# Kernel tuning notes

Measured on AMD Instinct MI355X. Metric: run time of the kernel, lower is better.

Reference implementation:

```python
import jax, jax.numpy as jnp
import numpy as np

N, E = 100000, 1600000
DIMS = [128, 64, 64, 64, 32]  # in, hid, hid, hid, out
NEG_SLOPE = 0.2               # GATv2Conv default negative_slope
ELU_ALPHA_OUT = float(DIMS[-1])  # nn.ELU(out_channels): alpha = out_channels


def setup_inputs() -> dict:
    key = jax.random.key(0)
    ks = jax.random.split(key, 16)
    inp = {
        "x": jax.random.normal(ks[0], (N, DIMS[0]), dtype=jnp.float32),
        "edge_index": jax.random.randint(ks[1], (2, E), 0, N, dtype=jnp.int64),
    }
    ki = 2
    for i in range(4):
        fin, fout = DIMS[i], DIMS[i + 1]
        s = 1.0 / np.sqrt(fin)
        inp[f"Wl{i+1}"] = jax.random.uniform(ks[ki], (fin, fout), jnp.float32, -s, s); ki += 1
        inp[f"Wr{i+1}"] = jax.random.uniform(ks[ki], (fin, fout), jnp.float32, -s, s); ki += 1
        inp[f"att{i+1}"] = jax.random.uniform(ks[ki], (fout,), jnp.float32, -s, s); ki += 1
    return inp


def gatv2_layer(x, src, dst, Wl, Wr, att):
    # single head, concat=False, no self-loops, no bias (per module config)
    xl = x @ Wl                                   # [N, F] source-side projection
    xr = x @ Wr                                   # [N, F] target-side projection
    e = jax.nn.leaky_relu(xl[src] + xr[dst], NEG_SLOPE)   # [E, F]
    score = e @ att                               # [E]
    # softmax over incoming edges of each destination node
    m = jax.ops.segment_max(score, dst, num_segments=N)    # [N]
    ex = jnp.exp(score - m[dst])                  # [E]
    denom = jax.ops.segment_sum(ex, dst, num_segments=N)   # [N]
    alpha = ex / (denom[dst] + 1e-16)             # [E]
    # scatter-add weighted source messages
    return jax.ops.segment_sum(xl[src] * alpha[:, None], dst, num_segments=N)


def reference(x, edge_index, Wl1, Wr1, att1, Wl2, Wr2, att2, Wl3, Wr3, att3, Wl4, Wr4, att4):
    src, dst = edge_index[0], edge_index[1]
    h = jax.nn.elu(gatv2_layer(x, src, dst, Wl1, Wr1, att1))
    h = jax.nn.elu(gatv2_layer(h, src, dst, Wl2, Wr2, att2))
    h = jax.nn.elu(gatv2_layer(h, src, dst, Wl3, Wr3, att3))
    h = gatv2_layer(h, src, dst, Wl4, Wr4, att4)
    # nn.ELU(out_channels) -> ELU with alpha = out_channels (faithful quirk)
    return jnp.where(h > 0, h, ELU_ALPHA_OUT * jnp.expm1(h))
```

## Files before the change

### kernel.cpp

```cpp
#include <hip/hip_runtime.h>
#include <math.h>

typedef __attribute__((ext_vector_type(8))) short bf16x8;
typedef __attribute__((ext_vector_type(4))) float f32x4;
typedef __attribute__((ext_vector_type(2))) _Float16 h2;

#define BSHIFT 7
#define CH 8192

__device__ inline unsigned short f32_to_bf16_bits(float f) {
    unsigned int u = __float_as_uint(f);
    unsigned int r = (u + 0x7fffu + ((u >> 16) & 1u)) >> 16;
    return (unsigned short)r;
}
__device__ inline float bf16_bits_to_f32(unsigned short h) {
    return __uint_as_float(((unsigned int)h) << 16);
}
__device__ inline h2 u2h(unsigned u) { return __builtin_bit_cast(h2, u); }
__device__ inline unsigned h2u(h2 h) { return __builtin_bit_cast(unsigned, h); }

#define SWZ_ADD(t, imm) \
    t += __int_as_float(__builtin_amdgcn_ds_swizzle(__float_as_int(t), imm))

__device__ inline float dot2acc(h2 a, h2 b, float c) {
#if defined(__has_builtin)
#if __has_builtin(__builtin_amdgcn_fdot2)
    return __builtin_amdgcn_fdot2(a, b, c, false);
#else
    return c + (float)a[0] * (float)b[0] + (float)a[1] * (float)b[1];
#endif
#else
    return c + (float)a[0] * (float)b[0] + (float)a[1] * (float)b[1];
#endif
}


__global__ __launch_bounds__(256) void bucket_hist(
    const int* __restrict__ dst, int* __restrict__ bcnt8, int E, int nb, int nbp)
{
    __shared__ int h[1024];
    for (int i = threadIdx.x; i < nb; i += 256) h[i] = 0;
    __syncthreads();
    int e0 = blockIdx.x * CH, e1 = min(e0 + CH, E);
    for (int e = e0 + (int)threadIdx.x; e < e1; e += 256)
        atomicAdd(&h[dst[e] >> BSHIFT], 1);
    __syncthreads();
    int* mycnt = bcnt8 + (blockIdx.x & 7) * nbp;
    for (int b = threadIdx.x; b < nb; b += 256) {
        int c = h[b];
        if (c) atomicAdd(&mycnt[b], c);
    }
}

__global__ void bucket_scan(const int* __restrict__ bcnt8, int* __restrict__ bbase,
                            int* __restrict__ bcur8, int* __restrict__ rowstart,
                            int nb, int nbp, int E, int N)
{
    __shared__ int sh[1024];
    int t = threadIdx.x;
    int g8[8];
    int tot = 0;
#pragma unroll
    for (int g = 0; g < 8; ++g) {
        int c = (t < nb) ? bcnt8[g * nbp + t] : 0;
        g8[g] = c; tot += c;
    }
    sh[t] = tot;
    __syncthreads();
    for (int d = 1; d < 1024; d <<= 1) {
        int a = (t >= d) ? sh[t - d] : 0;
        __syncthreads();
        sh[t] += a;
        __syncthreads();
    }
    int base = sh[t] - tot;
    if (t <= nb) bbase[t] = base;
    if (t < nb) {
        int run = base;
#pragma unroll
        for (int g = 0; g < 8; ++g) { bcur8[g * nbp + t] = run; run += g8[g]; }
    }
    if (t == 0) rowstart[N] = E;
}

__global__ __launch_bounds__(256) void bucket_scatter(
    const int* __restrict__ src, const int* __restrict__ dst,
    int* __restrict__ bcur8, unsigned* __restrict__ pairs, int E, int nb, int nbp)
{
    __shared__ int h[1024];
    for (int i = threadIdx.x; i < nb; i += 256) h[i] = 0;
    __syncthreads();
    int e0 = blockIdx.x * CH, e1 = min(e0 + CH, E);
    for (int e = e0 + (int)threadIdx.x; e < e1; e += 256)
        atomicAdd(&h[dst[e] >> BSHIFT], 1);
    __syncthreads();
    int* mycur = bcur8 + (blockIdx.x & 7) * nbp;
    for (int b = threadIdx.x; b < nb; b += 256) {
        int c = h[b];
        if (c) h[b] = atomicAdd(&mycur[b], c);
    }
    __syncthreads();
    for (int e = e0 + (int)threadIdx.x; e < e1; e += 256) {
        int d = dst[e];
        int pos = atomicAdd(&h[d >> BSHIFT], 1);
        pairs[pos] = ((unsigned)src[e] << BSHIFT) | (unsigned)(d & 127);
    }
}

__global__ __launch_bounds__(256) void bucket_finalize(
    const unsigned* __restrict__ pairs, const int* __restrict__ bbase,
    int* __restrict__ rowstart, int* __restrict__ csr_src, int N)
{
    __shared__ int h[128];
    __shared__ int sh[256];
    int b = blockIdx.x;
    int p0 = bbase[b], p1 = bbase[b + 1];
    int t = threadIdx.x;
    if (t < 128) h[t] = 0;
    __syncthreads();
    for (int e = p0 + t; e < p1; e += 256)
        atomicAdd(&h[pairs[e] & 127], 1);
    __syncthreads();
    int v = (t < 128) ? h[t] : 0;
    sh[t] = v;
    __syncthreads();
    for (int d = 1; d < 256; d <<= 1) {
        int a = (t >= d) ? sh[t - d] : 0;
        __syncthreads();
        sh[t] += a;
        __syncthreads();
    }
    if (t < 128) {
        int off = sh[t] - v;
        int node = (b << BSHIFT) + t;
        if (node < N) rowstart[node] = p0 + off;
        h[t] = p0 + off;
    }
    __syncthreads();
    for (int e = p0 + t; e < p1; e += 256) {
        unsigned pr = pairs[e];
        int pos = atomicAdd(&h[pr & 127], 1);
        csr_src[pos] = (int)(pr >> BSHIFT);
    }
}


__global__ void prepack_kernel(const float* __restrict__ Wl, const float* __restrict__ Wr,
                               unsigned short* __restrict__ pWl, unsigned short* __restrict__ pWr,
                               int FIN, int FOUT) {
    int NT = FOUT >> 4, NK = FIN >> 5;
    int part = NT * NK * 512;
    int i = blockIdx.x * blockDim.x + threadIdx.x;
    int m = i / part;
    if (m >= 2) return;
    int ii = i - m * part;
    int j = ii & 7;
    int lane = (ii >> 3) & 63;
    int rest = ii >> 9;
    int ks = rest % NK;
    int t = rest / NK;
    int k = ks * 32 + (lane >> 4) * 8 + j;
    int c = t * 16 + (lane & 15);
    const float* W = m ? Wr : Wl;
    unsigned short* P = m ? pWr : pWl;
    float w = W[(size_t)k * FOUT + c];
    unsigned short hi = f32_to_bf16_bits(w);
    unsigned short lo = f32_to_bf16_bits(w - bf16_bits_to_f32(hi));
    P[ii] = hi;
    P[part + ii] = lo;
}


template<int FIN, int FOUT>
__global__ __launch_bounds__(256) void proj_mfma_kernel(
    const float* __restrict__ x,
    const unsigned short* __restrict__ pWl, const unsigned short* __restrict__ pWr,
    const float* __restrict__ att,
    _Float16* __restrict__ xlh, _Float16* __restrict__ xrh,
    float* __restrict__ dl, float* __restrict__ dr, int n)
{
    constexpr int NT = FOUT >> 4;
    constexpr int NK = FIN >> 5;
    constexpr int PART = NT * NK * 512;
    const int wave = threadIdx.x >> 6;
    const int lane = threadIdx.x & 63;
    const int row0 = blockIdx.x * 64 + wave * 16;
    int arow = row0 + (lane & 15);
    if (arow >= n) arow = n - 1;
    const int khalf = lane >> 4;

    f32x4 accl[NT], accr[NT];
#pragma unroll
    for (int t = 0; t < NT; ++t) {
        accl[t] = (f32x4){0.f, 0.f, 0.f, 0.f};
        accr[t] = (f32x4){0.f, 0.f, 0.f, 0.f};
    }

    const float* xrow = x + (size_t)arow * FIN + khalf * 8;
#pragma unroll
    for (int ks = 0; ks < NK; ++ks) {
        float4 a0 = *(const float4*)(xrow + ks * 32);
        float4 a1 = *(const float4*)(xrow + ks * 32 + 4);
        float av[8] = {a0.x, a0.y, a0.z, a0.w, a1.x, a1.y, a1.z, a1.w};
        bf16x8 ah, al;
#pragma unroll
        for (int j = 0; j < 8; ++j) {
            unsigned short h = f32_to_bf16_bits(av[j]);
            ah[j] = (short)h;
            al[j] = (short)f32_to_bf16_bits(av[j] - bf16_bits_to_f32(h));
        }
#pragma unroll
        for (int t = 0; t < NT; ++t) {
            const unsigned short* bpl = pWl + ((size_t)(t * NK + ks) * 64 + lane) * 8;
            bf16x8 bh  = *(const bf16x8*)bpl;
            bf16x8 blo = *(const bf16x8*)(bpl + PART);
            accl[t] = __builtin_amdgcn_mfma_f32_16x16x32_bf16(ah, bh,  accl[t], 0, 0, 0);
            accl[t] = __builtin_amdgcn_mfma_f32_16x16x32_bf16(ah, blo, accl[t], 0, 0, 0);
            accl[t] = __builtin_amdgcn_mfma_f32_16x16x32_bf16(al, bh,  accl[t], 0, 0, 0);
            const unsigned short* bpr = pWr + ((size_t)(t * NK + ks) * 64 + lane) * 8;
            bh  = *(const bf16x8*)bpr;
            blo = *(const bf16x8*)(bpr + PART);
            accr[t] = __builtin_amdgcn_mfma_f32_16x16x32_bf16(ah, bh,  accr[t], 0, 0, 0);
            accr[t] = __builtin_amdgcn_mfma_f32_16x16x32_bf16(ah, blo, accr[t], 0, 0, 0);
            accr[t] = __builtin_amdgcn_mfma_f32_16x16x32_bf16(al, bh,  accr[t], 0, 0, 0);
        }
    }

    const int orow0 = row0 + khalf * 4;
    const int colb = lane & 15;
    float attc[NT];
#pragma unroll
    for (int t = 0; t < NT; ++t) attc[t] = att[t * 16 + colb];

#pragma unroll
    for (int t = 0; t < NT; ++t) {
        int col = t * 16 + colb;
#pragma unroll
        for (int r = 0; r < 4; ++r) {
            int rr = orow0 + r;
            if (rr < n) {
                xlh[(size_t)rr * FOUT + col] = (_Float16)accl[t][r];
                xrh[(size_t)rr * FOUT + col] = (_Float16)accr[t][r];
            }
        }
    }
#pragma unroll
    for (int r = 0; r < 4; ++r) {
        float pl = 0.f, pr = 0.f;
#pragma unroll
        for (int t = 0; t < NT; ++t) { pl += accl[t][r] * attc[t]; pr += accr[t][r] * attc[t]; }
#pragma unroll
        for (int off = 1; off < 16; off <<= 1) {
            pl += __shfl_xor(pl, off);
            pr += __shfl_xor(pr, off);
        }
        int rr = orow0 + r;
        if (colb == 0 && rr < n) { dl[rr] = pl; dr[rr] = pr; }
    }
}


template<int F, int AMODE>
__global__ __launch_bounds__(256) void agg_kernel(
    const _Float16* __restrict__ xlh, const _Float16* __restrict__ xrh,
    const float* __restrict__ att,
    const float* __restrict__ dl, const float* __restrict__ dr,
    const int* __restrict__ rowstart, const int* __restrict__ csr_src,
    float* __restrict__ out, int n, int E)
{
    constexpr int LPE = F / 8;
    constexpr int LSH = (F == 64) ? 6 : 5;
    constexpr int NPG = 64 / LPE;

    int wv  = (blockIdx.x * blockDim.x + threadIdx.x) >> 6;
    int lane = threadIdx.x & 63;
    int grp = lane / LPE;
    int fl  = lane % LPE;
    int node = wv * NPG + grp;
    bool act = node < n;
    int nc = act ? node : 0;

    float4 xrraw = *(const float4*)(xrh + (((unsigned)nc << LSH) + fl * 8));
    h2 xrv[4];
#pragma unroll
    for (int j = 0; j < 4; ++j) xrv[j] = u2h(((const unsigned*)&xrraw)[j]);
    h2 atth[4];
#pragma unroll
    for (int j = 0; j < 4; ++j) {
        atth[j][0] = (_Float16)att[fl * 8 + 2 * j];
        atth[j][1] = (_Float16)att[fl * 8 + 2 * j + 1];
    }
    float cdr = 0.6f * dr[nc];

    int s0 = rowstart[nc];
    int s1 = act ? rowstart[nc + 1] : s0;
    int s1c = min(max(s1 - 1, s0), E - 1);

    float m = -1e30f, mth = -1e30f, ssum = 0.f;
    float o[8];
#pragma unroll
    for (int j = 0; j < 8; ++j) o[j] = 0.f;

    int ia = s0, ib = s0 + 1;
    int sva = csr_src[min(ia, s1c)];
    int svb = csr_src[min(ib, s1c)];
    float dla = dl[sva], dlb = dl[svb];
    float4 rawa = *(const float4*)(xlh + (((unsigned)sva << LSH) + fl * 8));
    float4 rawb = *(const float4*)(xlh + (((unsigned)svb << LSH) + fl * 8));

    while (ia < s1) {
        int nia = ia + 2, nib = ib + 2;
        int nsva = csr_src[min(nia, s1c)];
        int nsvb = csr_src[min(nib, s1c)];
        float ndla = dl[nsva], ndlb = dl[nsvb];
        float4 nrawa = *(const float4*)(xlh + (((unsigned)nsva << LSH) + fl * 8));
        float4 nrawb = *(const float4*)(xlh + (((unsigned)nsvb << LSH) + fl * 8));

        h2 a[4], b[4];
#pragma unroll
        for (int j = 0; j < 4; ++j) {
            a[j] = u2h(((const unsigned*)&rawa)[j]);
            b[j] = u2h(((const unsigned*)&rawb)[j]);
        }

        bool vb = ib < s1;
        float ta = 0.f, tb = 0.f;
#pragma unroll
        for (int j = 0; j < 4; ++j) {
            h2 ea = a[j] + xrv[j];
            h2 eb = b[j] + xrv[j];
            ea = u2h(h2u(ea) & 0x7FFF7FFFu);
            eb = u2h(h2u(eb) & 0x7FFF7FFFu);
            ta = dot2acc(atth[j], ea, ta);
            tb = dot2acc(atth[j], eb, tb);
        }
        SWZ_ADD(ta, 0x041F); SWZ_ADD(tb, 0x041F);
        SWZ_ADD(ta, 0x081F); SWZ_ADD(tb, 0x081F);
        if (LPE == 8) { SWZ_ADD(ta, 0x101F); SWZ_ADD(tb, 0x101F); }

        float pa = 0.6f * dla + cdr + 0.4f * ta;
        float pb = vb ? (0.6f * dlb + cdr + 0.4f * tb) : -1e30f;

        float pm = fmaxf(pa, pb);
        if (pm > mth) {
            float c = __expf(m - pm);
            ssum *= c;
#pragma unroll
            for (int j = 0; j < 8; ++j) o[j] *= c;
            m = pm; mth = pm + 8.0f;
        }
        float wa = __expf(pa - m);
        float wb = __expf(pb - m);
        ssum += wa + wb;
#pragma unroll
        for (int j = 0; j < 4; ++j) {
            o[2 * j]     += wa * (float)a[j][0] + wb * (float)b[j][0];
            o[2 * j + 1] += wa * (float)a[j][1] + wb * (float)b[j][1];
        }

        ia = nia; ib = nib;
        dla = ndla; dlb = ndlb; rawa = nrawa; rawb = nrawb;
    }

    float inv = 1.f / (ssum + 1e-16f);
    float res[8];
#pragma unroll
    for (int j = 0; j < 8; ++j) {
        float r = o[j] * inv;
        if (AMODE == 1) r = (r > 0.f) ? r : expm1f(r);
        else            r = (r > 0.f) ? r : 32.f * expm1f(r);
        res[j] = r;
    }
    if (act) {
        float* op = out + (((unsigned)node << LSH) + fl * 8);
        *(float4*)op       = (float4){res[0], res[1], res[2], res[3]};
        *(float4*)(op + 4) = (float4){res[4], res[5], res[6], res[7]};
    }
}


extern "C" void kernel_launch(void* const* d_in, const int* in_sizes, int n_in,
                              void* d_out, int out_size, void* d_ws, size_t ws_size,
                              hipStream_t stream) {
    const float* x    = (const float*)d_in[0];
    const int*   ei   = (const int*)d_in[1];
    const float* Wl1  = (const float*)d_in[2];
    const float* Wr1  = (const float*)d_in[3];
    const float* att1 = (const float*)d_in[4];
    const float* Wl2  = (const float*)d_in[5];
    const float* Wr2  = (const float*)d_in[6];
    const float* att2 = (const float*)d_in[7];
    const float* Wl3  = (const float*)d_in[8];
    const float* Wr3  = (const float*)d_in[9];
    const float* att3 = (const float*)d_in[10];
    const float* Wl4  = (const float*)d_in[11];
    const float* Wr4  = (const float*)d_in[12];
    const float* att4 = (const float*)d_in[13];

    const int N = in_sizes[0] / 128;
    const int E = in_sizes[1] / 2;
    const int* src = ei;
    const int* dst = ei + E;

    const int nb  = (N + 127) >> BSHIFT;
    const int nbp = (nb + 15) & ~15;

    char* w = (char*)d_ws;
    size_t off = 0;
    auto take = [&](size_t bytes) -> void* {
        void* p = w + off;
        off = (off + bytes + 255) & ~(size_t)255;
        return p;
    };
    int* bcnt8    = (int*)take((size_t)8 * nbp * 4);
    int* bcur8    = (int*)take((size_t)8 * nbp * 4);
    int* bbase    = (int*)take((size_t)(nb + 1) * 4);
    int* rowstart = (int*)take((size_t)(N + 1) * 4);
    int* csr_src  = (int*)take((size_t)E * 4);
    float* dl = (float*)take((size_t)N * 4);
    float* dr = (float*)take((size_t)N * 4);
    _Float16* xlh = (_Float16*)take((size_t)N * 64 * 2);
    _Float16* xrh = (_Float16*)take((size_t)N * 64 * 2);
    float* hA = (float*)take((size_t)N * 64 * 4);
    float* hB = (float*)take((size_t)N * 64 * 4);
    unsigned short* pWl1 = (unsigned short*)take(2 * 4 * 4 * 512 * 2);
    unsigned short* pWr1 = (unsigned short*)take(2 * 4 * 4 * 512 * 2);
    unsigned short* pWl2 = (unsigned short*)take(2 * 4 * 2 * 512 * 2);
    unsigned short* pWr2 = (unsigned short*)take(2 * 4 * 2 * 512 * 2);
    unsigned short* pWl3 = (unsigned short*)take(2 * 4 * 2 * 512 * 2);
    unsigned short* pWr3 = (unsigned short*)take(2 * 4 * 2 * 512 * 2);
    unsigned short* pWl4 = (unsigned short*)take(2 * 2 * 2 * 512 * 2);
    unsigned short* pWr4 = (unsigned short*)take(2 * 2 * 2 * 512 * 2);
    unsigned* pairs = (unsigned*)hA;
    float* outf = (float*)d_out;

    hipMemsetAsync(bcnt8, 0, (size_t)8 * nbp * 4, stream);

    prepack_kernel<<<(2 * 4 * 4 * 512 + 255) / 256, 256, 0, stream>>>(Wl1, Wr1, pWl1, pWr1, 128, 64);
    prepack_kernel<<<(2 * 4 * 2 * 512 + 255) / 256, 256, 0, stream>>>(Wl2, Wr2, pWl2, pWr2, 64, 64);
    prepack_kernel<<<(2 * 4 * 2 * 512 + 255) / 256, 256, 0, stream>>>(Wl3, Wr3, pWl3, pWr3, 64, 64);
    prepack_kernel<<<(2 * 2 * 2 * 512 + 255) / 256, 256, 0, stream>>>(Wl4, Wr4, pWl4, pWr4, 64, 32);

    int kgrid = (E + CH - 1) / CH;
    bucket_hist<<<kgrid, 256, 0, stream>>>(dst, bcnt8, E, nb, nbp);
    bucket_scan<<<1, 1024, 0, stream>>>(bcnt8, bbase, bcur8, rowstart, nb, nbp, E, N);
    bucket_scatter<<<kgrid, 256, 0, stream>>>(src, dst, bcur8, pairs, E, nb, nbp);
    bucket_finalize<<<nb, 256, 0, stream>>>(pairs, bbase, rowstart, csr_src, N);

    int pblk = (N + 63) / 64;
    int agg64 = (N + 31) / 32;
    int agg32 = (N + 63) / 64;

    proj_mfma_kernel<128, 64><<<pblk, 256, 0, stream>>>(x, pWl1, pWr1, att1, xlh, xrh, dl, dr, N);
    agg_kernel<64, 1><<<agg64, 256, 0, stream>>>(xlh, xrh, att1, dl, dr, rowstart, csr_src, hA, N, E);

    proj_mfma_kernel<64, 64><<<pblk, 256, 0, stream>>>(hA, pWl2, pWr2, att2, xlh, xrh, dl, dr, N);
    agg_kernel<64, 1><<<agg64, 256, 0, stream>>>(xlh, xrh, att2, dl, dr, rowstart, csr_src, hB, N, E);

    proj_mfma_kernel<64, 64><<<pblk, 256, 0, stream>>>(hB, pWl3, pWr3, att3, xlh, xrh, dl, dr, N);
    agg_kernel<64, 1><<<agg64, 256, 0, stream>>>(xlh, xrh, att3, dl, dr, rowstart, csr_src, hA, N, E);

    proj_mfma_kernel<64, 32><<<pblk, 256, 0, stream>>>(hA, pWl4, pWr4, att4, xlh, xrh, dl, dr, N);
    agg_kernel<32, 2><<<agg32, 256, 0, stream>>>(xlh, xrh, att4, dl, dr, rowstart, csr_src, outf, N, E);
}
```

Baseline: 304.6 us.

## Sort aggregation nodes by in-degree and deepen edge gather prefetch

Adds a counting sort of nodes by in-degree (histogram, scan, scatter) and has each aggregation wave process nodes in that permuted order. Nodes sharing a wave then have similar edge counts, which reduces lane divergence in the per-node edge loop. The edge loop also prefetches two edge pairs ahead instead of one, to hide gather latency. In exchange it adds three small preprocessing kernels and an indirection, and writes to the output and reads of per-node data become non-contiguous. The deeper prefetch also raises register pressure.

```diff
diff --git a/kernel.cpp b/kernel.cpp
--- a/kernel.cpp
+++ b/kernel.cpp
@@ -141,6 +141,37 @@
         unsigned pr = pairs[e];
         int pos = atomicAdd(&h[pr & 127], 1);
         csr_src[pos] = (int)(pr >> BSHIFT);
+    }
+}
+
+
+__global__ void deg_hist(const int* __restrict__ rowstart, int* __restrict__ dhist, int N) {
+    int i = blockIdx.x * blockDim.x + threadIdx.x;
+    if (i < N) atomicAdd(&dhist[min(rowstart[i + 1] - rowstart[i], 255)], 1);
+}
+
+__global__ void deg_scan(const int* __restrict__ dhist, int* __restrict__ dcur) {
+    __shared__ int sh[256];
+    int t = threadIdx.x;
+    int v = dhist[t];
+    sh[t] = v;
+    __syncthreads();
+    for (int d = 1; d < 256; d <<= 1) {
+        int a = (t >= d) ? sh[t - d] : 0;
+        __syncthreads();
+        sh[t] += a;
+        __syncthreads();
+    }
+    dcur[t] = sh[t] - v;
+}
+
+__global__ void deg_scatter(const int* __restrict__ rowstart, int* __restrict__ dcur,
+                            int* __restrict__ perm, int N) {
+    int i = blockIdx.x * blockDim.x + threadIdx.x;
+    if (i < N) {
+        int d = min(rowstart[i + 1] - rowstart[i], 255);
+        int r = atomicAdd(&dcur[d], 1);
+        perm[r] = i;
     }
 }
 
@@ -266,6 +297,7 @@
     const float* __restrict__ att,
     const float* __restrict__ dl, const float* __restrict__ dr,
     const int* __restrict__ rowstart, const int* __restrict__ csr_src,
+    const int* __restrict__ perm,
     float* __restrict__ out, int n, int E)
 {
     constexpr int LPE = F / 8;
@@ -276,11 +308,11 @@
     int lane = threadIdx.x & 63;
     int grp = lane / LPE;
     int fl  = lane % LPE;
-    int node = wv * NPG + grp;
-    bool act = node < n;
-    int nc = act ? node : 0;
-
-    float4 xrraw = *(const float4*)(xrh + (((unsigned)nc << LSH) + fl * 8));
+    int idx = wv * NPG + grp;
+    bool act = idx < n;
+    int node = act ? perm[idx] : 0;
+
+    float4 xrraw = *(const float4*)(xrh + (((unsigned)node << LSH) + fl * 8));
     h2 xrv[4];
 #pragma unroll
     for (int j = 0; j < 4; ++j) xrv[j] = u2h(((const unsigned*)&xrraw)[j]);
@@ -290,10 +322,10 @@
         atth[j][0] = (_Float16)att[fl * 8 + 2 * j];
         atth[j][1] = (_Float16)att[fl * 8 + 2 * j + 1];
     }
-    float cdr = 0.6f * dr[nc];
-
-    int s0 = rowstart[nc];
-    int s1 = act ? rowstart[nc + 1] : s0;
+    float cdr = 0.6f * dr[node];
+
+    int s0 = rowstart[node];
+    int s1 = act ? rowstart[node + 1] : s0;
     int s1c = min(max(s1 - 1, s0), E - 1);
 
     float m = -1e30f, mth = -1e30f, ssum = 0.f;
@@ -301,29 +333,34 @@
 #pragma unroll
     for (int j = 0; j < 8; ++j) o[j] = 0.f;
 
-    int ia = s0, ib = s0 + 1;
-    int sva = csr_src[min(ia, s1c)];
-    int svb = csr_src[min(ib, s1c)];
-    float dla = dl[sva], dlb = dl[svb];
-    float4 rawa = *(const float4*)(xlh + (((unsigned)sva << LSH) + fl * 8));
-    float4 rawb = *(const float4*)(xlh + (((unsigned)svb << LSH) + fl * 8));
-
-    while (ia < s1) {
-        int nia = ia + 2, nib = ib + 2;
-        int nsva = csr_src[min(nia, s1c)];
-        int nsvb = csr_src[min(nib, s1c)];
-        float ndla = dl[nsva], ndlb = dl[nsvb];
-        float4 nrawa = *(const float4*)(xlh + (((unsigned)nsva << LSH) + fl * 8));
-        float4 nrawb = *(const float4*)(xlh + (((unsigned)nsvb << LSH) + fl * 8));
+    int i0 = s0;
+    int sa = csr_src[min(s0,     s1c)];
+    int sb = csr_src[min(s0 + 1, s1c)];
+    float da0 = dl[sa], db0 = dl[sb];
+    float4 ra0 = *(const float4*)(xlh + (((unsigned)sa << LSH) + fl * 8));
+    float4 rb0 = *(const float4*)(xlh + (((unsigned)sb << LSH) + fl * 8));
+    sa = csr_src[min(s0 + 2, s1c)];
+    sb = csr_src[min(s0 + 3, s1c)];
+    float da1 = dl[sa], db1 = dl[sb];
+    float4 ra1 = *(const float4*)(xlh + (((unsigned)sa << LSH) + fl * 8));
+    float4 rb1 = *(const float4*)(xlh + (((unsigned)sb << LSH) + fl * 8));
+
+    while (i0 < s1) {
+        int p2 = i0 + 4;
+        int sa2 = csr_src[min(p2,     s1c)];
+        int sb2 = csr_src[min(p2 + 1, s1c)];
+        float da2 = dl[sa2], db2 = dl[sb2];
+        float4 ra2 = *(const float4*)(xlh + (((unsigned)sa2 << LSH) + fl * 8));
+        float4 rb2 = *(const float4*)(xlh + (((unsigned)sb2 << LSH) + fl * 8));
 
         h2 a[4], b[4];
 #pragma unroll
         for (int j = 0; j < 4; ++j) {
-            a[j] = u2h(((const unsigned*)&rawa)[j]);
-            b[j] = u2h(((const unsigned*)&rawb)[j]);
-        }
-
-        bool vb = ib < s1;
+            a[j] = u2h(((const unsigned*)&ra0)[j]);
+            b[j] = u2h(((const unsigned*)&rb0)[j]);
+        }
+
+        bool vb = (i0 + 1) < s1;
         float ta = 0.f, tb = 0.f;
 #pragma unroll
         for (int j = 0; j < 4; ++j) {
@@ -338,8 +375,8 @@
         SWZ_ADD(ta, 0x081F); SWZ_ADD(tb, 0x081F);
         if (LPE == 8) { SWZ_ADD(ta, 0x101F); SWZ_ADD(tb, 0x101F); }
 
-        float pa = 0.6f * dla + cdr + 0.4f * ta;
-        float pb = vb ? (0.6f * dlb + cdr + 0.4f * tb) : -1e30f;
+        float pa = 0.6f * da0 + cdr + 0.4f * ta;
+        float pb = vb ? (0.6f * db0 + cdr + 0.4f * tb) : -1e30f;
 
         float pm = fmaxf(pa, pb);
         if (pm > mth) {
@@ -358,8 +395,9 @@
             o[2 * j + 1] += wa * (float)a[j][1] + wb * (float)b[j][1];
         }
 
-        ia = nia; ib = nib;
-        dla = ndla; dlb = ndlb; rawa = nrawa; rawb = nrawb;
+        i0 += 2;
+        da0 = da1; db0 = db1; ra0 = ra1; rb0 = rb1;
+        da1 = da2; db1 = db2; ra1 = ra2; rb1 = rb2;
     }
 
     float inv = 1.f / (ssum + 1e-16f);
@@ -417,6 +455,9 @@
     int* bbase    = (int*)take((size_t)(nb + 1) * 4);
     int* rowstart = (int*)take((size_t)(N + 1) * 4);
     int* csr_src  = (int*)take((size_t)E * 4);
+    int* dhist    = (int*)take(256 * 4);
+    int* dcur     = (int*)take(256 * 4);
+    int* perm     = (int*)take((size_t)N * 4);
     float* dl = (float*)take((size_t)N * 4);
     float* dr = (float*)take((size_t)N * 4);
     _Float16* xlh = (_Float16*)take((size_t)N * 64 * 2);
@@ -435,6 +476,7 @@
     float* outf = (float*)d_out;
 
     hipMemsetAsync(bcnt8, 0, (size_t)8 * nbp * 4, stream);
+    hipMemsetAsync(dhist, 0, 256 * 4, stream);
 
     prepack_kernel<<<(2 * 4 * 4 * 512 + 255) / 256, 256, 0, stream>>>(Wl1, Wr1, pWl1, pWr1, 128, 64);
     prepack_kernel<<<(2 * 4 * 2 * 512 + 255) / 256, 256, 0, stream>>>(Wl2, Wr2, pWl2, pWr2, 64, 64);
@@ -447,19 +489,24 @@
     bucket_scatter<<<kgrid, 256, 0, stream>>>(src, dst, bcur8, pairs, E, nb, nbp);
     bucket_finalize<<<nb, 256, 0, stream>>>(pairs, bbase, rowstart, csr_src, N);
 
+    int ngrid = (N + 255) / 256;
+    deg_hist<<<ngrid, 256, 0, stream>>>(rowstart, dhist, N);
+    deg_scan<<<1, 256, 0, stream>>>(dhist, dcur);
+    deg_scatter<<<ngrid, 256, 0, stream>>>(rowstart, dcur, perm, N);
+
     int pblk = (N + 63) / 64;
     int agg64 = (N + 31) / 32;
     int agg32 = (N + 63) / 64;
 
     proj_mfma_kernel<128, 64><<<pblk, 256, 0, stream>>>(x, pWl1, pWr1, att1, xlh, xrh, dl, dr, N);
-    agg_kernel<64, 1><<<agg64, 256, 0, stream>>>(xlh, xrh, att1, dl, dr, rowstart, csr_src, hA, N, E);
+    agg_kernel<64, 1><<<agg64, 256, 0, stream>>>(xlh, xrh, att1, dl, dr, rowstart, csr_src, perm, hA, N, E);
 
     proj_mfma_kernel<64, 64><<<pblk, 256, 0, stream>>>(hA, pWl2, pWr2, att2, xlh, xrh, dl, dr, N);
-    agg_kernel<64, 1><<<agg64, 256, 0, stream>>>(xlh, xrh, att2, dl, dr, rowstart, csr_src, hB, N, E);
+    agg_kernel<64, 1><<<agg64, 256, 0, stream>>>(xlh, xrh, att2, dl, dr, rowstart, csr_src, perm, hB, N, E);
 
     proj_mfma_kernel<64, 64><<<pblk, 256, 0, stream>>>(hB, pWl3, pWr3, att3, xlh, xrh, dl, dr, N);
-    agg_kernel<64, 1><<<agg64, 256, 0, stream>>>(xlh, xrh, att3, dl, dr, rowstart, csr_src, hA, N, E);
+    agg_kernel<64, 1><<<agg64, 256, 0, stream>>>(xlh, xrh, att3, dl, dr, rowstart, csr_src, perm, hA, N, E);
 
     proj_mfma_kernel<64, 32><<<pblk, 256, 0, stream>>>(hA, pWl4, pWr4, att4, xlh, xrh, dl, dr, N);
-    agg_kernel<32, 2><<<agg32, 256, 0, stream>>>(xlh, xrh, att4, dl, dr, rowstart, csr_src, outf, N, E);
-}
+    agg_kernel<32, 2><<<agg32, 256, 0, stream>>>(xlh, xrh, att4, dl, dr, rowstart, csr_src, perm, outf, N, E);
+}
```

After: 845.3 us. +177.5%, slower.

## Deepen gather prefetch pipeline in GAT aggregation loop to two stages

Applied to the files above, without the earlier changes.

Restructures the per-destination edge loop into a software pipeline that keeps two pairs of gathered source rows in flight and prefetches CSR source indices further ahead. The aim is to hide the latency of the dependent index-then-row gather chain behind the attention and softmax arithmetic. In exchange it uses more registers, which may reduce occupancy, and it issues more speculative clamped loads for nodes with few edges.

```diff
diff --git a/kernel.cpp b/kernel.cpp
--- a/kernel.cpp
+++ b/kernel.cpp
@@ -301,66 +301,89 @@
 #pragma unroll
     for (int j = 0; j < 8; ++j) o[j] = 0.f;
 
-    int ia = s0, ib = s0 + 1;
-    int sva = csr_src[min(ia, s1c)];
-    int svb = csr_src[min(ib, s1c)];
-    float dla = dl[sva], dlb = dl[svb];
-    float4 rawa = *(const float4*)(xlh + (((unsigned)sva << LSH) + fl * 8));
-    float4 rawb = *(const float4*)(xlh + (((unsigned)svb << LSH) + fl * 8));
-
-    while (ia < s1) {
-        int nia = ia + 2, nib = ib + 2;
-        int nsva = csr_src[min(nia, s1c)];
-        int nsvb = csr_src[min(nib, s1c)];
-        float ndla = dl[nsva], ndlb = dl[nsvb];
-        float4 nrawa = *(const float4*)(xlh + (((unsigned)nsva << LSH) + fl * 8));
-        float4 nrawb = *(const float4*)(xlh + (((unsigned)nsvb << LSH) + fl * 8));
-
-        h2 a[4], b[4];
-#pragma unroll
-        for (int j = 0; j < 4; ++j) {
-            a[j] = u2h(((const unsigned*)&rawa)[j]);
-            b[j] = u2h(((const unsigned*)&rawb)[j]);
-        }
-
-        bool vb = ib < s1;
-        float ta = 0.f, tb = 0.f;
-#pragma unroll
-        for (int j = 0; j < 4; ++j) {
-            h2 ea = a[j] + xrv[j];
-            h2 eb = b[j] + xrv[j];
-            ea = u2h(h2u(ea) & 0x7FFF7FFFu);
-            eb = u2h(h2u(eb) & 0x7FFF7FFFu);
-            ta = dot2acc(atth[j], ea, ta);
-            tb = dot2acc(atth[j], eb, tb);
-        }
-        SWZ_ADD(ta, 0x041F); SWZ_ADD(tb, 0x041F);
-        SWZ_ADD(ta, 0x081F); SWZ_ADD(tb, 0x081F);
-        if (LPE == 8) { SWZ_ADD(ta, 0x101F); SWZ_ADD(tb, 0x101F); }
-
-        float pa = 0.6f * dla + cdr + 0.4f * ta;
-        float pb = vb ? (0.6f * dlb + cdr + 0.4f * tb) : -1e30f;
-
-        float pm = fmaxf(pa, pb);
-        if (pm > mth) {
-            float c = __expf(m - pm);
-            ssum *= c;
-#pragma unroll
-            for (int j = 0; j < 8; ++j) o[j] *= c;
-            m = pm; mth = pm + 8.0f;
-        }
-        float wa = __expf(pa - m);
-        float wb = __expf(pb - m);
-        ssum += wa + wb;
-#pragma unroll
-        for (int j = 0; j < 4; ++j) {
-            o[2 * j]     += wa * (float)a[j][0] + wb * (float)b[j][0];
-            o[2 * j + 1] += wa * (float)a[j][1] + wb * (float)b[j][1];
-        }
-
-        ia = nia; ib = nib;
-        dla = ndla; dlb = ndlb; rawa = nrawa; rawb = nrawb;
-    }
+    int cA0 = csr_src[min(s0,     s1c)];
+    int cB0 = csr_src[min(s0 + 1, s1c)];
+    int cA1 = csr_src[min(s0 + 2, s1c)];
+    int cB1 = csr_src[min(s0 + 3, s1c)];
+    float4 rA0 = *(const float4*)(xlh + (((unsigned)cA0 << LSH) + fl * 8));
+    float4 rB0 = *(const float4*)(xlh + (((unsigned)cB0 << LSH) + fl * 8));
+    float  dA0 = dl[cA0], dB0 = dl[cB0];
+    float4 rA1 = *(const float4*)(xlh + (((unsigned)cA1 << LSH) + fl * 8));
+    float4 rB1 = *(const float4*)(xlh + (((unsigned)cB1 << LSH) + fl * 8));
+    float  dA1 = dl[cA1], dB1 = dl[cB1];
+    int fA0 = csr_src[min(s0 + 4, s1c)];
+    int fB0 = csr_src[min(s0 + 5, s1c)];
+    int fA1 = csr_src[min(s0 + 6, s1c)];
+    int fB1 = csr_src[min(s0 + 7, s1c)];
+
+    int i0 = s0;
+
+#define AGG_COMPUTE(RA, RB, DA, DB)                                          \
+    {                                                                        \
+        h2 a[4], b[4];                                                       \
+        _Pragma("unroll")                                                    \
+        for (int j = 0; j < 4; ++j) {                                        \
+            a[j] = u2h(((const unsigned*)&RA)[j]);                           \
+            b[j] = u2h(((const unsigned*)&RB)[j]);                           \
+        }                                                                    \
+        bool vb = (i0 + 1) < s1;                                             \
+        float ta = 0.f, tb = 0.f;                                            \
+        _Pragma("unroll")                                                    \
+        for (int j = 0; j < 4; ++j) {                                        \
+            h2 ea = a[j] + xrv[j];                                           \
+            h2 eb = b[j] + xrv[j];                                           \
+            ea = u2h(h2u(ea) & 0x7FFF7FFFu);                                 \
+            eb = u2h(h2u(eb) & 0x7FFF7FFFu);                                 \
+            ta = dot2acc(atth[j], ea, ta);                                   \
+            tb = dot2acc(atth[j], eb, tb);                                   \
+        }                                                                    \
+        SWZ_ADD(ta, 0x041F); SWZ_ADD(tb, 0x041F);                            \
+        SWZ_ADD(ta, 0x081F); SWZ_ADD(tb, 0x081F);                            \
+        if (LPE == 8) { SWZ_ADD(ta, 0x101F); SWZ_ADD(tb, 0x101F); }          \
+        float pa = 0.6f * DA + cdr + 0.4f * ta;                              \
+        float pb = vb ? (0.6f * DB + cdr + 0.4f * tb) : -1e30f;              \
+        float pm = fmaxf(pa, pb);                                            \
+        if (pm > mth) {                                                      \
+            float c = __expf(m - pm);                                        \
+            ssum *= c;                                                       \
+            _Pragma("unroll")                                                \
+            for (int j = 0; j < 8; ++j) o[j] *= c;                           \
+            m = pm; mth = pm + 8.0f;                                         \
+        }                                                                    \
+        float wa = __expf(pa - m);                                           \
+        float wb = __expf(pb - m);                                           \
+        ssum += wa + wb;                                                     \
+        _Pragma("unroll")                                                    \
+        for (int j = 0; j < 4; ++j) {                                        \
+            o[2 * j]     += wa * (float)a[j][0] + wb * (float)b[j][0];       \
+            o[2 * j + 1] += wa * (float)a[j][1] + wb * (float)b[j][1];       \
+        }                                                                    \
+    }
+
+    while (i0 < s1) {
+        {
+            int cA2 = fA0, cB2 = fB0;
+            fA0 = csr_src[min(i0 + 8, s1c)];
+            fB0 = csr_src[min(i0 + 9, s1c)];
+            AGG_COMPUTE(rA0, rB0, dA0, dB0);
+            rA0 = *(const float4*)(xlh + (((unsigned)cA2 << LSH) + fl * 8));
+            rB0 = *(const float4*)(xlh + (((unsigned)cB2 << LSH) + fl * 8));
+            dA0 = dl[cA2]; dB0 = dl[cB2];
+        }
+        i0 += 2;
+        if (i0 >= s1) break;
+        {
+            int cA2 = fA1, cB2 = fB1;
+            fA1 = csr_src[min(i0 + 8, s1c)];
+            fB1 = csr_src[min(i0 + 9, s1c)];
+            AGG_COMPUTE(rA1, rB1, dA1, dB1);
+            rA1 = *(const float4*)(xlh + (((unsigned)cA2 << LSH) + fl * 8));
+            rB1 = *(const float4*)(xlh + (((unsigned)cB2 << LSH) + fl * 8));
+            dA1 = dl[cA2]; dB1 = dl[cB2];
+        }
+        i0 += 2;
+    }
+#undef AGG_COMPUTE
 
     float inv = 1.f / (ssum + 1e-16f);
     float res[8];
```

Result: faster. 295.5 us (-3.0%).
